# Optimization experiments

Hardware: AMD Instinct MI355X
Metric: run time of the kernel (lower is better)

Reference implementation:

```python
import jax, jax.numpy as jnp
import numpy as np

L = 16384      # sequence length
D_IN = 512     # d_input
D_H = 1024     # d_hidden
D_OUT = 512    # d_output
R_MIN = 0.0
R_MAX = 0.99
MAX_PHASE = np.pi


def setup_inputs() -> dict:
    key = jax.random.key(0)
    k_nu, k_th, k_x, k_bre, k_bim, k_cre, k_cim, k_d = jax.random.split(key, 8)
    # nu_init with parametrization='exp'
    u_nu = jax.random.uniform(k_nu, (D_H,), dtype=jnp.float32)
    nu = jnp.sqrt(u_nu * (R_MAX ** 2 - R_MIN ** 2) + R_MIN ** 2)
    u_theta = jax.random.uniform(k_th, (D_H,), dtype=jnp.float32, minval=-MAX_PHASE, maxval=MAX_PHASE)
    theta = jnp.mod(u_theta, 2 * jnp.pi)
    lamb = jnp.stack([jnp.log(-jnp.log(nu)), jnp.log(theta)], axis=0)  # [2, D_H]
    # gamma_init with parametrization='exp': nu = exp(-exp(lamb[0]))
    nu_eff = jnp.exp(-jnp.exp(lamb[0]))
    gamma = jnp.log(jnp.sqrt(1.0 - jnp.abs(nu_eff) ** 2))  # [D_H]
    # matrix_init: normal / sqrt(shape[0])
    B_re = jax.random.normal(k_bre, (D_H, D_IN), dtype=jnp.float32) / jnp.sqrt(D_H)
    B_im = jax.random.normal(k_bim, (D_H, D_IN), dtype=jnp.float32) / jnp.sqrt(D_H)
    C_re = jax.random.normal(k_cre, (D_OUT, D_H), dtype=jnp.float32) / jnp.sqrt(D_OUT)
    C_im = jax.random.normal(k_cim, (D_OUT, D_H), dtype=jnp.float32) / jnp.sqrt(D_OUT)
    D = jax.random.normal(k_d, (D_OUT, D_IN), dtype=jnp.float32) / jnp.sqrt(D_OUT)
    inputs = jax.random.normal(k_x, (L, D_IN), dtype=jnp.float32)
    return {"inputs": inputs, "lamb": lamb, "gamma": gamma,
            "B_re": B_re, "B_im": B_im, "C_re": C_re, "C_im": C_im, "D": D}


def _binary_operator_diag(q_i, q_j):
    A_i, b_i = q_i
    A_j, b_j = q_j
    return (A_j * A_i, A_j * b_i + b_j)


def reference(inputs, lamb, gamma, B_re, B_im, C_re, C_im, D):
    # parametrization='exp': lambda = exp(-exp(nu_log) + i*exp(theta_log))
    diag_lambda = jnp.exp(-jnp.exp(lamb[0]) + 1j * jnp.exp(lamb[1]))  # [D_H] complex64
    # which_gamma='learned', exp param: scale rows of B by exp(gamma)
    B_norm = jnp.exp(gamma)[:, None] * (B_re + 1j * B_im)             # [D_H, D_IN]
    # Bu_t = B_norm @ x_t for all t, as one GEMM: [L, D_H] complex
    Bu = inputs.astype(B_norm.dtype) @ B_norm.T
    Lambda_elements = jnp.broadcast_to(diag_lambda[None, :], Bu.shape)
    # diagonal linear recurrence h_t = lambda*h_{t-1} + Bu_t via parallel scan
    _, h = jax.lax.associative_scan(_binary_operator_diag, (Lambda_elements, Bu))
    C = C_re + 1j * C_im
    # y_t = Re[C h_t] + D x_t
    outputs = jnp.real(h @ C.T) + inputs @ D.T  # [L, D_OUT]
    return outputs
```

## Files before the change

### kernel.cpp

```cpp
#include <hip/hip_runtime.h>

__device__ __forceinline__ unsigned short f2b(float f) {
    unsigned int u = __builtin_bit_cast(unsigned int, f);
    unsigned int r = (u + 0x7FFFu + ((u >> 16) & 1u)) >> 16;
    return (unsigned short)r;
}
__device__ __forceinline__ float b2f(unsigned short s) {
    unsigned int u = ((unsigned int)s) << 16;
    return __builtin_bit_cast(float, u);
}

typedef __attribute__((ext_vector_type(8))) short short8;
typedef __attribute__((ext_vector_type(4))) float float4v;

#define GLD16(g, l) __builtin_amdgcn_global_load_lds(                          \
    (const __attribute__((address_space(1))) unsigned int*)(g),                \
    (__attribute__((address_space(3))) unsigned int*)(l), 16, 0, 0)

#define WAIT_VMN(n)  __builtin_amdgcn_s_waitcnt(0x0F70 | (n))
#define SB()         __builtin_amdgcn_sched_barrier(0)
#define BAR()        __builtin_amdgcn_s_barrier()

#define SEQLEN 16384
#define NCHUNK 512
#define TCHUNK 32
#define LDH 2560

__global__ void prep_all(const float* __restrict__ x,
                         const float* __restrict__ B_re, const float* __restrict__ B_im,
                         const float* __restrict__ gamma,
                         const float* __restrict__ C_re, const float* __restrict__ C_im,
                         const float* __restrict__ Dm,
                         unsigned short* __restrict__ Hcat,
                         unsigned short* __restrict__ Bcat,
                         unsigned short* __restrict__ CW) {
    int b = blockIdx.x;
    if (b < 8192) {
        int id = b * 256 + threadIdx.x;
        int t = id >> 7;
        int k4 = (id & 127) << 2;
        float4 v = *(const float4*)(x + (long)t * 512 + k4);
        ushort4 o;
        o.x = f2b(v.x); o.y = f2b(v.y); o.z = f2b(v.z); o.w = f2b(v.w);
        *(ushort4*)(Hcat + (long)t * LDH + 2048 + k4) = o;
    } else if (b < 9216) {
        int id = (b - 8192) * 256 + threadIdx.x;
        int n = id >> 7;
        int k4 = (id & 127) << 2;
        const float* src = (n < 1024) ? (B_re + (long)n * 512) : (B_im + (long)(n - 1024) * 512);
        float g = expf(gamma[n & 1023]);
        float4 v = *(const float4*)(src + k4);
        ushort4 o;
        o.x = f2b(v.x * g); o.y = f2b(v.y * g); o.z = f2b(v.z * g); o.w = f2b(v.w * g);
        *(ushort4*)(Bcat + (long)n * 512 + k4) = o;
    } else {
        int id = (b - 9216) * 256 + threadIdx.x;
        int o = id / 640;
        int j4 = (id - o * 640) << 2;
        float4 v; float sgn = 1.0f;
        if (j4 < 1024) {
            v = *(const float4*)(C_re + (long)o * 1024 + j4);
        } else if (j4 < 2048) {
            v = *(const float4*)(C_im + (long)o * 1024 + (j4 - 1024));
            sgn = -1.0f;
        } else {
            v = *(const float4*)(Dm + (long)o * 512 + (j4 - 2048));
        }
        ushort4 w;
        w.x = f2b(v.x * sgn); w.y = f2b(v.y * sgn); w.z = f2b(v.z * sgn); w.w = f2b(v.w * sgn);
        *(ushort4*)(CW + (long)o * 2560 + j4) = w;
    }
}

template <bool OUT_BF16>
__launch_bounds__(256, 2)
__global__ void gemm_w4(const unsigned short* __restrict__ A, int lda,
                        const unsigned short* __restrict__ B, int ldb,
                        void* __restrict__ Cout, int ldc, int Ktot,
                        int nbx_shift) {
    __shared__ unsigned short sm[3][12288] __attribute__((aligned(16)));
    const int tid  = threadIdx.x;
    const int lane = tid & 63;
    const int wid  = tid >> 6;
    const int wr   = wid >> 1;
    const int wc   = wid & 1;

    const int bid = blockIdx.x;
    const int xcd = bid & 7;
    const int g   = bid >> 3;
    const int bx  = g & ((1 << nbx_shift) - 1);
    const int by  = xcd * (gridDim.x >> (3 + nbx_shift)) + (g >> nbx_shift);
    const long m0 = (long)by * 256;
    const long n0 = (long)bx * 128;

    const int sr = lane >> 2;
    const int sc = (((lane & 3) ^ ((lane >> 3) & 3)) << 3);
    const unsigned short* Agl = A + (m0 + sr) * (long)lda + sc;
    const unsigned short* Bgl = B + (n0 + sr) * (long)ldb + sc;

    const int fr   = lane & 15;
    const int koff = (((lane >> 4) ^ ((fr >> 1) & 3)) << 3);

    float4v acc[8][4] = {};
    short8 fa[8], fb[4];

    auto stage = [&](unsigned short* buf, long kt) {
#pragma unroll
        for (int i = 0; i < 4; i++)
            GLD16(Agl + (long)(wid * 64 + i * 16) * lda + kt, buf + (wid * 4 + i) * 512);
#pragma unroll
        for (int j = 0; j < 2; j++)
            GLD16(Bgl + (long)(wid * 32 + j * 16) * ldb + kt, buf + 8192 + (wid * 2 + j) * 512);
    };
    auto ldAall = [&](const unsigned short* buf) {
#pragma unroll
        for (int i = 0; i < 8; i++)
            fa[i] = *(const short8*)(buf + (wr * 128 + i * 16 + fr) * 32 + koff);
    };
    auto ldB2 = [&](const unsigned short* buf, int nbase) {
#pragma unroll
        for (int j = 0; j < 2; j++)
            fb[nbase + j] = *(const short8*)(buf + 8192 + (wc * 64 + (nbase + j) * 16 + fr) * 32 + koff);
    };
    auto mfma16 = [&](int nbase) {
        __builtin_amdgcn_s_setprio(1);
#pragma unroll
        for (int i = 0; i < 8; i++)
#pragma unroll
            for (int j = 0; j < 2; j++)
                acc[i][nbase + j] = __builtin_amdgcn_mfma_f32_16x16x32_bf16(
                    fa[i], fb[nbase + j], acc[i][nbase + j], 0, 0, 0);
        __builtin_amdgcn_s_setprio(0);
    };

    const int nk = Ktot >> 5;

    unsigned short* p0 = sm[0];
    unsigned short* p1 = sm[1];
    unsigned short* p2 = sm[2];
    stage(p0, 0);
    stage(p1, 32);
    WAIT_VMN(6);
    SB(); BAR(); SB();

    for (int t = 0; t < nk; ++t) {
        const bool st = (t + 2 < nk);
        ldAall(p0); ldB2(p0, 0);
        SB(); BAR(); SB();
        mfma16(0);
        SB(); BAR(); SB();
        ldB2(p0, 2);
        if (st) stage(p2, (long)(t + 2) * 32);
        SB(); BAR(); SB();
        mfma16(2);
        if (st)              WAIT_VMN(6);
        else if (t + 1 < nk) WAIT_VMN(0);
        SB(); BAR(); SB();
        unsigned short* tmp = p0; p0 = p1; p1 = p2; p2 = tmp;
    }

    const int er = (lane >> 4) * 4;
    const int ec = lane & 15;
#pragma unroll
    for (int mi = 0; mi < 8; mi++) {
#pragma unroll
        for (int r = 0; r < 4; r++) {
            long grow = m0 + wr * 128 + mi * 16 + er + r;
#pragma unroll
            for (int nj = 0; nj < 4; nj++) {
                long gcol = n0 + wc * 64 + nj * 16 + ec;
                float v = acc[mi][nj][r];
                if (OUT_BF16)
                    ((unsigned short*)Cout)[grow * ldc + gcol] = f2b(v);
                else
                    ((float*)Cout)[grow * ldc + gcol] = v;
            }
        }
    }
}

__global__ void scan_ends(const unsigned short* __restrict__ Hcat,
                          const float* __restrict__ lamb,
                          float* __restrict__ E) {
    const int chunk = blockIdx.x;
    const int ch = threadIdx.x << 2;
    float lre[4], lim[4];
#pragma unroll
    for (int i = 0; i < 4; i++) {
        float nu = expf(-expf(lamb[ch + i]));
        float th = expf(lamb[1024 + ch + i]);
        lre[i] = nu * cosf(th);
        lim[i] = nu * sinf(th);
    }
    float hr[4] = {0, 0, 0, 0}, hi[4] = {0, 0, 0, 0};
    const unsigned short* base = Hcat + (long)chunk * TCHUNK * LDH + ch;
#pragma unroll 4
    for (int t = 0; t < TCHUNK; t++) {
        ushort4 br = *(const ushort4*)(base + (long)t * LDH);
        ushort4 bi = *(const ushort4*)(base + (long)t * LDH + 1024);
        float brf[4] = {b2f(br.x), b2f(br.y), b2f(br.z), b2f(br.w)};
        float bif[4] = {b2f(bi.x), b2f(bi.y), b2f(bi.z), b2f(bi.w)};
#pragma unroll
        for (int i = 0; i < 4; i++) {
            float nr = fmaf(lre[i], hr[i], fmaf(-lim[i], hi[i], brf[i]));
            float ni = fmaf(lre[i], hi[i], fmaf(lim[i], hr[i], bif[i]));
            hr[i] = nr; hi[i] = ni;
        }
    }
    float* Ec = E + (long)chunk * 2048 + ch;
#pragma unroll
    for (int i = 0; i < 4; i++) {
        Ec[i] = hr[i];
        Ec[1024 + i] = hi[i];
    }
}

__global__ void carry(const float* __restrict__ lamb, const float* __restrict__ E,
                      float* __restrict__ Kc) {
    const int lane = threadIdx.x & 63;
    const int ch = blockIdx.x * 4 + (threadIdx.x >> 6);
    double nu = exp(-exp((double)lamb[ch]));
    double th = exp((double)lamb[1024 + ch]);
    double lr = nu * cos(th), li = nu * sin(th);
#pragma unroll
    for (int i = 0; i < 5; i++) {
        double rr = lr * lr - li * li;
        double ii = 2.0 * lr * li;
        lr = rr; li = ii;
    }
    const float tre = (float)lr, tim = (float)li;
    double ar = lr, ai = li;
#pragma unroll
    for (int i = 0; i < 3; i++) {
        double rr = ar * ar - ai * ai;
        double ii = 2.0 * ar * ai;
        ar = rr; ai = ii;
    }
    float Ar = (float)ar, Ai = (float)ai;

    const int c0 = lane * 8;
    float er[8], ei[8];
#pragma unroll
    for (int j = 0; j < 8; j++) {
        er[j] = E[(long)(c0 + j) * 2048 + ch];
        ei[j] = E[(long)(c0 + j) * 2048 + 1024 + ch];
    }
    float hr = 0.0f, hi = 0.0f;
#pragma unroll
    for (int j = 0; j < 8; j++) {
        float nr = fmaf(tre, hr, fmaf(-tim, hi, er[j]));
        float ni = fmaf(tre, hi, fmaf(tim, hr, ei[j]));
        hr = nr; hi = ni;
    }
#pragma unroll
    for (int o = 1; o < 64; o <<= 1) {
        float pr = __shfl_up(hr, o);
        float pi = __shfl_up(hi, o);
        float qr = __shfl_up(Ar, o);
        float qi = __shfl_up(Ai, o);
        if (lane >= o) {
            float nr = fmaf(Ar, pr, fmaf(-Ai, pi, hr));
            float ni = fmaf(Ar, pi, fmaf(Ai, pr, hi));
            hr = nr; hi = ni;
            float nar = Ar * qr - Ai * qi;
            float nai = Ar * qi + Ai * qr;
            Ar = nar; Ai = nai;
        }
    }
    float sr = __shfl_up(hr, 1);
    float si = __shfl_up(hi, 1);
    if (lane == 0) { sr = 0.0f; si = 0.0f; }
#pragma unroll
    for (int j = 0; j < 8; j++) {
        Kc[(long)(c0 + j) * 2048 + ch] = sr;
        Kc[(long)(c0 + j) * 2048 + 1024 + ch] = si;
        float nr = fmaf(tre, sr, fmaf(-tim, si, er[j]));
        float ni = fmaf(tre, si, fmaf(tim, sr, ei[j]));
        sr = nr; si = ni;
    }
}

__global__ void scan_apply(unsigned short* __restrict__ Hcat,
                           const float* __restrict__ lamb,
                           const float* __restrict__ Kc) {
    const int chunk = blockIdx.x;
    const int ch = threadIdx.x << 2;
    float lre[4], lim[4];
#pragma unroll
    for (int i = 0; i < 4; i++) {
        float nu = expf(-expf(lamb[ch + i]));
        float th = expf(lamb[1024 + ch + i]);
        lre[i] = nu * cosf(th);
        lim[i] = nu * sinf(th);
    }
    float hr[4], hi[4];
#pragma unroll
    for (int i = 0; i < 4; i++) {
        hr[i] = Kc[(long)chunk * 2048 + ch + i];
        hi[i] = Kc[(long)chunk * 2048 + 1024 + ch + i];
    }
    unsigned short* base = Hcat + (long)chunk * TCHUNK * LDH + ch;
#pragma unroll 4
    for (int t = 0; t < TCHUNK; t++) {
        ushort4 br = *(const ushort4*)(base + (long)t * LDH);
        ushort4 bi = *(const ushort4*)(base + (long)t * LDH + 1024);
        float brf[4] = {b2f(br.x), b2f(br.y), b2f(br.z), b2f(br.w)};
        float bif[4] = {b2f(bi.x), b2f(bi.y), b2f(bi.z), b2f(bi.w)};
#pragma unroll
        for (int i = 0; i < 4; i++) {
            float nr = fmaf(lre[i], hr[i], fmaf(-lim[i], hi[i], brf[i]));
            float ni = fmaf(lre[i], hi[i], fmaf(lim[i], hr[i], bif[i]));
            hr[i] = nr; hi[i] = ni;
        }
        ushort4 orv, oiv;
        orv.x = f2b(hr[0]); orv.y = f2b(hr[1]); orv.z = f2b(hr[2]); orv.w = f2b(hr[3]);
        oiv.x = f2b(hi[0]); oiv.y = f2b(hi[1]); oiv.z = f2b(hi[2]); oiv.w = f2b(hi[3]);
        *(ushort4*)(base + (long)t * LDH) = orv;
        *(ushort4*)(base + (long)t * LDH + 1024) = oiv;
    }
}

extern "C" void kernel_launch(void* const* d_in, const int* in_sizes, int n_in,
                              void* d_out, int out_size, void* d_ws, size_t ws_size,
                              hipStream_t stream) {
    const float* x     = (const float*)d_in[0];
    const float* lamb  = (const float*)d_in[1];
    const float* gamma = (const float*)d_in[2];
    const float* B_re  = (const float*)d_in[3];
    const float* B_im  = (const float*)d_in[4];
    const float* C_re  = (const float*)d_in[5];
    const float* C_im  = (const float*)d_in[6];
    const float* Dm    = (const float*)d_in[7];

    char* ws = (char*)d_ws;
    unsigned short* Hcat = (unsigned short*)ws;
    float* E  = (float*)(ws + 83886080);
    float* Kc = E + (long)NCHUNK * 2048;
    unsigned short* Bcat = (unsigned short*)((char*)Kc + 4194304);
    unsigned short* CW   = Bcat + (long)2048 * 512;

    prep_all<<<10496, 256, 0, stream>>>(x, B_re, B_im, gamma, C_re, C_im, Dm, Hcat, Bcat, CW);
    gemm_w4<true><<<1024, 256, 0, stream>>>(Hcat + 2048, LDH, Bcat, 512, Hcat, LDH, 512,
                                            4);
    scan_ends<<<NCHUNK, 256, 0, stream>>>(Hcat, lamb, E);
    carry<<<256, 256, 0, stream>>>(lamb, E, Kc);
    scan_apply<<<NCHUNK, 256, 0, stream>>>(Hcat, lamb, Kc);
    gemm_w4<false><<<256, 256, 0, stream>>>(Hcat, LDH, CW, 2560, (float*)d_out, 512, 2560,
                                            2);
}
```

Measured before the change: 243.3 us.

## Shrink GEMM tile to 128x128 with a 4-stage single-barrier pipeline

Changes the bf16 GEMM block tile from 256x128 to 128x128, halving per-wave accumulators and fragments, and doubles the grid sizes to match. The LDS ring grows from three to four buffers with a prefetch depth of three, and each K step now needs one barrier instead of four. The goal is more blocks and occupancy, particularly for the second GEMM, which previously ran only 256 blocks, and less barrier overhead. The trade-off is lower reuse per loaded tile, which raises global and L2 traffic.

```diff
diff --git a/kernel.cpp b/kernel.cpp
--- a/kernel.cpp
+++ b/kernel.cpp
@@ -78,7 +78,7 @@
                         const unsigned short* __restrict__ B, int ldb,
                         void* __restrict__ Cout, int ldc, int Ktot,
                         int nbx_shift) {
-    __shared__ unsigned short sm[3][12288] __attribute__((aligned(16)));
+    __shared__ unsigned short sm[4][8192] __attribute__((aligned(16)));
     const int tid  = threadIdx.x;
     const int lane = tid & 63;
     const int wid  = tid >> 6;
@@ -90,7 +90,7 @@
     const int g   = bid >> 3;
     const int bx  = g & ((1 << nbx_shift) - 1);
     const int by  = xcd * (gridDim.x >> (3 + nbx_shift)) + (g >> nbx_shift);
-    const long m0 = (long)by * 256;
+    const long m0 = (long)by * 128;
     const long n0 = (long)bx * 128;
 
     const int sr = lane >> 2;
@@ -101,71 +101,59 @@
     const int fr   = lane & 15;
     const int koff = (((lane >> 4) ^ ((fr >> 1) & 3)) << 3);
 
-    float4v acc[8][4] = {};
-    short8 fa[8], fb[4];
+    float4v acc[4][4] = {};
+    short8 fa[4], fb[4];
 
     auto stage = [&](unsigned short* buf, long kt) {
 #pragma unroll
+        for (int i = 0; i < 2; i++)
+            GLD16(Agl + (long)(wid * 32 + i * 16) * lda + kt, buf + (wid * 2 + i) * 512);
+#pragma unroll
+        for (int i = 0; i < 2; i++)
+            GLD16(Bgl + (long)(wid * 32 + i * 16) * ldb + kt, buf + 4096 + (wid * 2 + i) * 512);
+    };
+    auto ldfrags = [&](const unsigned short* buf) {
+#pragma unroll
         for (int i = 0; i < 4; i++)
-            GLD16(Agl + (long)(wid * 64 + i * 16) * lda + kt, buf + (wid * 4 + i) * 512);
-#pragma unroll
-        for (int j = 0; j < 2; j++)
-            GLD16(Bgl + (long)(wid * 32 + j * 16) * ldb + kt, buf + 8192 + (wid * 2 + j) * 512);
+            fa[i] = *(const short8*)(buf + (wr * 64 + i * 16 + fr) * 32 + koff);
+#pragma unroll
+        for (int j = 0; j < 4; j++)
+            fb[j] = *(const short8*)(buf + 4096 + (wc * 64 + j * 16 + fr) * 32 + koff);
     };
-    auto ldAall = [&](const unsigned short* buf) {
-#pragma unroll
-        for (int i = 0; i < 8; i++)
-            fa[i] = *(const short8*)(buf + (wr * 128 + i * 16 + fr) * 32 + koff);
-    };
-    auto ldB2 = [&](const unsigned short* buf, int nbase) {
-#pragma unroll
-        for (int j = 0; j < 2; j++)
-            fb[nbase + j] = *(const short8*)(buf + 8192 + (wc * 64 + (nbase + j) * 16 + fr) * 32 + koff);
-    };
-    auto mfma16 = [&](int nbase) {
+
+    const int nk = Ktot >> 5;
+
+    stage(sm[0], 0);
+    stage(sm[1], 32);
+    stage(sm[2], 64);
+    WAIT_VMN(8);
+    SB(); BAR(); SB();
+
+    for (int t = 0; t < nk; ++t) {
+        ldfrags(sm[t & 3]);
+        if (t + 3 < nk) stage(sm[(t + 3) & 3], (long)(t + 3) * 32);
+        SB();
         __builtin_amdgcn_s_setprio(1);
 #pragma unroll
-        for (int i = 0; i < 8; i++)
-#pragma unroll
-            for (int j = 0; j < 2; j++)
-                acc[i][nbase + j] = __builtin_amdgcn_mfma_f32_16x16x32_bf16(
-                    fa[i], fb[nbase + j], acc[i][nbase + j], 0, 0, 0);
+        for (int i = 0; i < 4; i++)
+#pragma unroll
+            for (int j = 0; j < 4; j++)
+                acc[i][j] = __builtin_amdgcn_mfma_f32_16x16x32_bf16(
+                    fa[i], fb[j], acc[i][j], 0, 0, 0);
         __builtin_amdgcn_s_setprio(0);
-    };
-
-    const int nk = Ktot >> 5;
-
-    unsigned short* p0 = sm[0];
-    unsigned short* p1 = sm[1];
-    unsigned short* p2 = sm[2];
-    stage(p0, 0);
-    stage(p1, 32);
-    WAIT_VMN(6);
-    SB(); BAR(); SB();
-
-    for (int t = 0; t < nk; ++t) {
-        const bool st = (t + 2 < nk);
-        ldAall(p0); ldB2(p0, 0);
+        if (t + 4 <= nk)      WAIT_VMN(8);
+        else if (t + 3 == nk) WAIT_VMN(4);
+        else if (t + 2 == nk) WAIT_VMN(0);
         SB(); BAR(); SB();
-        mfma16(0);
-        SB(); BAR(); SB();
-        ldB2(p0, 2);
-        if (st) stage(p2, (long)(t + 2) * 32);
-        SB(); BAR(); SB();
-        mfma16(2);
-        if (st)              WAIT_VMN(6);
-        else if (t + 1 < nk) WAIT_VMN(0);
-        SB(); BAR(); SB();
-        unsigned short* tmp = p0; p0 = p1; p1 = p2; p2 = tmp;
     }
 
     const int er = (lane >> 4) * 4;
     const int ec = lane & 15;
 #pragma unroll
-    for (int mi = 0; mi < 8; mi++) {
+    for (int mi = 0; mi < 4; mi++) {
 #pragma unroll
         for (int r = 0; r < 4; r++) {
-            long grow = m0 + wr * 128 + mi * 16 + er + r;
+            long grow = m0 + wr * 64 + mi * 16 + er + r;
 #pragma unroll
             for (int nj = 0; nj < 4; nj++) {
                 long gcol = n0 + wc * 64 + nj * 16 + ec;
@@ -340,11 +328,11 @@
     unsigned short* CW   = Bcat + (long)2048 * 512;
 
     prep_all<<<10496, 256, 0, stream>>>(x, B_re, B_im, gamma, C_re, C_im, Dm, Hcat, Bcat, CW);
-    gemm_w4<true><<<1024, 256, 0, stream>>>(Hcat + 2048, LDH, Bcat, 512, Hcat, LDH, 512,
+    gemm_w4<true><<<2048, 256, 0, stream>>>(Hcat + 2048, LDH, Bcat, 512, Hcat, LDH, 512,
                                             4);
     scan_ends<<<NCHUNK, 256, 0, stream>>>(Hcat, lamb, E);
     carry<<<256, 256, 0, stream>>>(lamb, E, Kc);
     scan_apply<<<NCHUNK, 256, 0, stream>>>(Hcat, lamb, Kc);
-    gemm_w4<false><<<256, 256, 0, stream>>>(Hcat, LDH, CW, 2560, (float*)d_out, 512, 2560,
+    gemm_w4<false><<<512, 256, 0, stream>>>(Hcat, LDH, CW, 2560, (float*)d_out, 512, 2560,
                                             2);
 }
```

New measurement: 247.9 us. About the same (+1.9%).
